# Kernel optimization log

Measured on AMD Instinct MI355X. Metric: run time of the kernel, lower is better.

Reference implementation:

```python
import jax, jax.numpy as jnp
import numpy as np

N = 524288   # tokens (accounts)
D = 9        # num_prop_size
E = 2        # expert_size
H = 128      # expert MLP hidden
M = 32       # moe_out
O = 2        # output_size
K = 1        # top-k
LOSS_COF = 0.01
EPS = 1e-10


def setup_inputs() -> dict:
    key = jax.random.key(0)
    ks = jax.random.split(key, 10)
    f32 = jnp.float32
    return {
        "num_prop": jax.random.normal(ks[0], (N, D), f32),
        "cat_prop": jax.random.normal(ks[1], (N, 3), f32),
        "w_gate": jax.random.normal(ks[2], (D, E), f32) * 0.1,
        "W1": jax.random.normal(ks[3], (E, D, H), f32) * 0.1,
        "b1": jax.random.normal(ks[4], (E, H), f32) * 0.01,
        "W2": jax.random.normal(ks[5], (E, H, M), f32) * 0.1,
        "b2": jax.random.normal(ks[6], (E, M), f32) * 0.01,
        "Wout": jax.random.normal(ks[7], (M, O), f32) * 0.1,
        "bout": jax.random.normal(ks[8], (O,), f32) * 0.01,
        "k": K,
    }


def _cv_squared(x):
    # torch: x.var() (unbiased) / (x.mean()**2 + eps)
    return jnp.var(x, ddof=1) / (jnp.mean(x) ** 2 + EPS)


def reference(num_prop, cat_prop, w_gate, W1, b1, W2, b2, Wout, bout, k):
    x = num_prop                                   # eval mode: dropout = identity
    n, e = x.shape[0], w_gate.shape[1]

    # --- top-k gating (eval: clean logits, no noise) ---
    logits = x @ w_gate                            # [N, E]
    top_logits, top_idx = jax.lax.top_k(logits, min(k + 1, e))
    top_k_gates = jax.nn.softmax(top_logits[:, :k], axis=1)   # [N, k]
    rows = jnp.arange(n)[:, None]
    gates = jnp.zeros_like(logits).at[rows, top_idx[:, :k]].set(top_k_gates)  # [N, E]

    importance = gates.sum(axis=0)                 # [E]
    load = (gates > 0).astype(jnp.float32).sum(axis=0)  # [E]
    loss = (_cv_squared(importance) + _cv_squared(load)) * LOSS_COF

    # --- experts: per-expert 2-layer MLP, computed dense (E=2) then gated combine ---
    h = jax.nn.relu(jnp.einsum("nd,edh->neh", x, W1) + b1)    # [N, E, H]
    y_e = jnp.einsum("neh,ehm->nem", h, W2) + b2              # [N, E, M]
    y = jnp.einsum("ne,nem->nm", gates, y_e)                  # [N, M]

    out = y @ Wout + bout                                     # [N, O]
    return (out, loss)
```

## Files before the change

kernel.cpp:

```cpp
#include <hip/hip_runtime.h>
#include <hip/hip_bf16.h>

#define NTOK 524288
#define TPB  256
#define NBLK (NTOK / TPB)

__device__ __forceinline__ float bf2f(unsigned short u) {
    union { unsigned int i; float f; } v;
    v.i = ((unsigned int)u) << 16;
    return v.f;
}

__device__ __forceinline__ float ldq(const void* p, int i, bool f32) {
    if (f32) return ((const float*)p)[i];
    return bf2f(((const unsigned short*)p)[i]);
}

__global__ void prep_kernel(const void* __restrict__ num_prop,
                            const void* __restrict__ wgate,
                            const void* __restrict__ W1,
                            const void* __restrict__ b1,
                            const void* __restrict__ W2,
                            const void* __restrict__ b2,
                            const void* __restrict__ Wout,
                            const void* __restrict__ bout,
                            unsigned int* __restrict__ cnt1,
                            int* __restrict__ flag,
                            float* __restrict__ bpp,
                            float* __restrict__ wgf,
                            float* __restrict__ wpack)
{
    __shared__ int sflag;
    const int t = threadIdx.x;
    if (t == 0) {
        const unsigned short* u = (const unsigned short*)num_prop;
        int f = 0;
        for (int i = 0; i < 72; ++i) {
            int e = (u[i] >> 7) & 0xFF;
            if (e < 64 || e > 191) f = 1;
        }
        sflag = f; *flag = f; *cnt1 = 0u;
    }
    __syncthreads();
    const bool f32 = (sflag != 0);

    if (t < 18) wgf[t] = ldq(wgate, t, f32);

    if (t < 4) {
        int e = t >> 1, o = t & 1;
        float acc = ldq(bout, o, f32);
        for (int m = 0; m < 32; ++m)
            acc += ldq(b2, e * 32 + m, f32) * ldq(Wout, m * 2 + o, f32);
        bpp[t] = acc;
    }

    const int e = t >> 7;
    const int j = t & 127;
    float p0 = 0.f, p1 = 0.f;
    for (int m = 0; m < 32; ++m) {
        float w = ldq(W2, (e * 128 + j) * 32 + m, f32);
        p0 += w * ldq(Wout, m * 2 + 0, f32);
        p1 += w * ldq(Wout, m * 2 + 1, f32);
    }
    float* dst = wpack + j * 24 + e * 12;
    #pragma unroll
    for (int d = 0; d < 9; ++d)
        dst[d] = ldq(W1, (e * 9 + d) * 128 + j, f32);
    dst[9]  = ldq(b1, e * 128 + j, f32);
    dst[10] = p0;
    dst[11] = p1;
}

__global__ __launch_bounds__(TPB, 8)
void moe_main(const void* __restrict__ xg,
              const int* __restrict__ flag,
              const float* __restrict__ wgf,
              const float* __restrict__ bpp,
              const float* __restrict__ wpack,
              unsigned int* __restrict__ cnt1,
              float2* __restrict__ out)
{
    __shared__ float xs[TPB * 9];
    __shared__ unsigned int cblk;
    const int tid = threadIdx.x;
    if (tid == 0) cblk = 0u;

    const bool f32 = (*flag) != 0;
    const int base = blockIdx.x * (TPB * 9);
    if (f32) {
        const float* xf = (const float*)xg;
        for (int i = tid; i < TPB * 9; i += TPB)
            xs[i] = xf[base + i];
    } else {
        const unsigned short* xu = (const unsigned short*)xg;
        for (int i = tid; i < TPB * 9; i += TPB)
            xs[i] = bf2f(xu[base + i]);
    }
    __syncthreads();

    float x[9];
    #pragma unroll
    for (int d = 0; d < 9; ++d) x[d] = xs[tid * 9 + d];

    float l0 = 0.f, l1 = 0.f;
    #pragma unroll
    for (int d = 0; d < 9; ++d) {
        l0 = fmaf(x[d], wgf[d * 2 + 0], l0);
        l1 = fmaf(x[d], wgf[d * 2 + 1], l1);
    }
    const bool e1 = l1 > l0;

    unsigned long long bal = __ballot(e1);
    if ((tid & 63) == 0)
        atomicAdd(&cblk, (unsigned int)__popcll(bal));

    float a00 = bpp[0], a01 = bpp[1], a10 = bpp[2], a11 = bpp[3];

    #pragma unroll 4
    for (int j = 0; j < 128; ++j) {
        const float* wp = wpack + j * 24;
        float h0 = wp[9], h1 = wp[21];
        #pragma unroll
        for (int d = 0; d < 9; ++d) {
            h0 = fmaf(x[d], wp[d],      h0);
            h1 = fmaf(x[d], wp[12 + d], h1);
        }
        h0 = fmaxf(h0, 0.f);
        h1 = fmaxf(h1, 0.f);
        a00 = fmaf(h0, wp[10], a00);
        a01 = fmaf(h0, wp[11], a01);
        a10 = fmaf(h1, wp[22], a10);
        a11 = fmaf(h1, wp[23], a11);
    }

    float2 o;
    o.x = e1 ? a10 : a00;
    o.y = e1 ? a11 : a01;
    out[blockIdx.x * TPB + tid] = o;

    __syncthreads();
    if (tid == 0) atomicAdd(cnt1, cblk);
}

__global__ void finalize_kernel(const unsigned int* __restrict__ cnt1,
                                float* __restrict__ loss_out)
{
    double c1 = (double)(*cnt1);
    double c0 = (double)NTOK - c1;
    double diff = c0 - c1;
    double mean = (double)NTOK * 0.5;
    double var  = 0.5 * diff * diff;
    double cv2  = var / (mean * mean + 1e-10);
    *loss_out = (float)(0.02 * cv2);
}

extern "C" void kernel_launch(void* const* d_in, const int* in_sizes, int n_in,
                              void* d_out, int out_size, void* d_ws, size_t ws_size,
                              hipStream_t stream) {
    const void* num_prop = d_in[0];
    const void* w_gate   = d_in[2];
    const void* W1       = d_in[3];
    const void* b1       = d_in[4];
    const void* W2       = d_in[5];
    const void* b2       = d_in[6];
    const void* Wout     = d_in[7];
    const void* bout     = d_in[8];

    char* ws = (char*)d_ws;
    unsigned int* cnt1 = (unsigned int*)ws;
    int* flag          = (int*)(ws + 8);
    float* bpp         = (float*)(ws + 16);
    float* wgf         = (float*)(ws + 64);
    float* wpack       = (float*)(ws + 192);

    float*  outf = (float*)d_out;
    float2* out2 = (float2*)d_out;

    hipLaunchKernelGGL(prep_kernel, dim3(1), dim3(256), 0, stream,
                       num_prop, w_gate, W1, b1, W2, b2, Wout, bout,
                       cnt1, flag, bpp, wgf, wpack);
    hipLaunchKernelGGL(moe_main, dim3(NBLK), dim3(TPB), 0, stream,
                       num_prop, flag, wgf, bpp, wpack, cnt1, out2);
    hipLaunchKernelGGL(finalize_kernel, dim3(1), dim3(1), 0, stream,
                       cnt1, outf + (size_t)NTOK * 2);
}
```

Before: 145.8 us.

## Sort tokens by expert within block to skip computing unused expert MLP

Tokens in each block are permuted by their top-1 expert through a ballot/mbcnt prefix, so most wavefronts hold tokens for a single expert and evaluate only that expert's MLP, roughly halving FLOPs. Mixed wavefronts fall back to computing both experts. The weight pack is split into per-expert contiguous arrays. The finalize kernel is folded into the main kernel with a last-block ticket counter, the input flag check is parallelised, and launch bounds drop to 6 blocks per SM. Risks are extra syncs, scattered output writes, and uniform weight loads from a different layout.

```diff
diff --git a/kernel.cpp b/kernel.cpp
--- a/kernel.cpp
+++ b/kernel.cpp
@@ -25,24 +25,24 @@
                             const void* __restrict__ Wout,
                             const void* __restrict__ bout,
                             unsigned int* __restrict__ cnt1,
+                            unsigned int* __restrict__ done,
                             int* __restrict__ flag,
                             float* __restrict__ bpp,
                             float* __restrict__ wgf,
                             float* __restrict__ wpack)
 {
-    __shared__ int sflag;
+    __shared__ int sbad;
     const int t = threadIdx.x;
-    if (t == 0) {
-        const unsigned short* u = (const unsigned short*)num_prop;
-        int f = 0;
-        for (int i = 0; i < 72; ++i) {
-            int e = (u[i] >> 7) & 0xFF;
-            if (e < 64 || e > 191) f = 1;
-        }
-        sflag = f; *flag = f; *cnt1 = 0u;
-    }
-    __syncthreads();
-    const bool f32 = (sflag != 0);
+    if (t == 0) { sbad = 0; *cnt1 = 0u; *done = 0u; }
+    __syncthreads();
+    if (t < 72) {
+        unsigned short u = ((const unsigned short*)num_prop)[t];
+        int e = (u >> 7) & 0xFF;
+        if (e < 64 || e > 191) sbad = 1;
+    }
+    __syncthreads();
+    const bool f32 = (sbad != 0);
+    if (t == 0) *flag = sbad;
 
     if (t < 18) wgf[t] = ldq(wgate, t, f32);
 
@@ -62,7 +62,7 @@
         p0 += w * ldq(Wout, m * 2 + 0, f32);
         p1 += w * ldq(Wout, m * 2 + 1, f32);
     }
-    float* dst = wpack + j * 24 + e * 12;
+    float* dst = wpack + e * 1536 + j * 12;
     #pragma unroll
     for (int d = 0; d < 9; ++d)
         dst[d] = ldq(W1, (e * 9 + d) * 128 + j, f32);
@@ -71,87 +71,125 @@
     dst[11] = p1;
 }
 
-__global__ __launch_bounds__(TPB, 8)
+__global__ __launch_bounds__(TPB, 6)
 void moe_main(const void* __restrict__ xg,
               const int* __restrict__ flag,
               const float* __restrict__ wgf,
               const float* __restrict__ bpp,
               const float* __restrict__ wpack,
               unsigned int* __restrict__ cnt1,
-              float2* __restrict__ out)
+              unsigned int* __restrict__ done,
+              float2* __restrict__ out,
+              float* __restrict__ loss_out)
 {
     __shared__ float xs[TPB * 9];
-    __shared__ unsigned int cblk;
-    const int tid = threadIdx.x;
-    if (tid == 0) cblk = 0u;
+    __shared__ unsigned short perm[TPB];
+    __shared__ int wcnt[4];
+    const int tid  = threadIdx.x;
+    const int lane = tid & 63;
+    const int wave = tid >> 6;
 
     const bool f32 = (*flag) != 0;
     const int base = blockIdx.x * (TPB * 9);
+    float xo[9];
     if (f32) {
-        const float* xf = (const float*)xg;
-        for (int i = tid; i < TPB * 9; i += TPB)
-            xs[i] = xf[base + i];
+        const float* xf = (const float*)xg + base + tid * 9;
+        #pragma unroll
+        for (int d = 0; d < 9; ++d) xo[d] = xf[d];
     } else {
-        const unsigned short* xu = (const unsigned short*)xg;
-        for (int i = tid; i < TPB * 9; i += TPB)
-            xs[i] = bf2f(xu[base + i]);
-    }
-    __syncthreads();
-
+        const unsigned short* xu = (const unsigned short*)xg + base + tid * 9;
+        #pragma unroll
+        for (int d = 0; d < 9; ++d) xo[d] = bf2f(xu[d]);
+    }
+    #pragma unroll
+    for (int d = 0; d < 9; ++d) xs[tid * 9 + d] = xo[d];
+
+    float l0 = 0.f, l1 = 0.f;
+    #pragma unroll
+    for (int d = 0; d < 9; ++d) {
+        l0 = fmaf(xo[d], wgf[d * 2 + 0], l0);
+        l1 = fmaf(xo[d], wgf[d * 2 + 1], l1);
+    }
+    const bool e1 = l1 > l0;
+
+    unsigned long long m1 = __ballot(e1);
+    int pre1 = __builtin_amdgcn_mbcnt_hi((unsigned)(m1 >> 32),
+               __builtin_amdgcn_mbcnt_lo((unsigned)m1, 0u));
+    if (lane == 0) wcnt[wave] = (int)__popcll(m1);
+    __syncthreads();
+    int w0 = wcnt[0], w1 = wcnt[1], w2 = wcnt[2], w3 = wcnt[3];
+    int c1_tot = w0 + w1 + w2 + w3;
+    int c0_tot = TPB - c1_tot;
+    int off1 = (wave > 0 ? w0 : 0) + (wave > 1 ? w1 : 0) + (wave > 2 ? w2 : 0);
+    int off0 = wave * 64 - off1;
+    int pos = e1 ? (c0_tot + off1 + pre1) : (off0 + (lane - pre1));
+    perm[pos] = (unsigned short)tid;
+    if (tid == 0) atomicAdd(cnt1, (unsigned int)c1_tot);
+    __syncthreads();
+
+    const int tok = perm[tid];
     float x[9];
     #pragma unroll
-    for (int d = 0; d < 9; ++d) x[d] = xs[tid * 9 + d];
-
-    float l0 = 0.f, l1 = 0.f;
-    #pragma unroll
-    for (int d = 0; d < 9; ++d) {
-        l0 = fmaf(x[d], wgf[d * 2 + 0], l0);
-        l1 = fmaf(x[d], wgf[d * 2 + 1], l1);
-    }
-    const bool e1 = l1 > l0;
-
-    unsigned long long bal = __ballot(e1);
-    if ((tid & 63) == 0)
-        atomicAdd(&cblk, (unsigned int)__popcll(bal));
-
-    float a00 = bpp[0], a01 = bpp[1], a10 = bpp[2], a11 = bpp[3];
-
-    #pragma unroll 4
-    for (int j = 0; j < 128; ++j) {
-        const float* wp = wpack + j * 24;
-        float h0 = wp[9], h1 = wp[21];
-        #pragma unroll
-        for (int d = 0; d < 9; ++d) {
-            h0 = fmaf(x[d], wp[d],      h0);
-            h1 = fmaf(x[d], wp[12 + d], h1);
+    for (int d = 0; d < 9; ++d) x[d] = xs[tok * 9 + d];
+    __syncthreads();
+
+    const bool my1 = (tid >= c0_tot);
+    unsigned long long bm = __ballot(my1);
+
+    float o0, o1;
+    if (bm == 0ull || bm == ~0ull) {
+        const int eb = (bm != 0ull) ? 1 : 0;
+        const float* wp = wpack + eb * 1536;
+        float a0 = bpp[eb * 2 + 0], a1 = bpp[eb * 2 + 1];
+        #pragma unroll 4
+        for (int j = 0; j < 128; ++j) {
+            const float* w = wp + j * 12;
+            float h = w[9];
+            #pragma unroll
+            for (int d = 0; d < 9; ++d) h = fmaf(x[d], w[d], h);
+            h = fmaxf(h, 0.f);
+            a0 = fmaf(h, w[10], a0);
+            a1 = fmaf(h, w[11], a1);
         }
-        h0 = fmaxf(h0, 0.f);
-        h1 = fmaxf(h1, 0.f);
-        a00 = fmaf(h0, wp[10], a00);
-        a01 = fmaf(h0, wp[11], a01);
-        a10 = fmaf(h1, wp[22], a10);
-        a11 = fmaf(h1, wp[23], a11);
-    }
-
-    float2 o;
-    o.x = e1 ? a10 : a00;
-    o.y = e1 ? a11 : a01;
-    out[blockIdx.x * TPB + tid] = o;
-
-    __syncthreads();
-    if (tid == 0) atomicAdd(cnt1, cblk);
-}
-
-__global__ void finalize_kernel(const unsigned int* __restrict__ cnt1,
-                                float* __restrict__ loss_out)
-{
-    double c1 = (double)(*cnt1);
-    double c0 = (double)NTOK - c1;
-    double diff = c0 - c1;
-    double mean = (double)NTOK * 0.5;
-    double var  = 0.5 * diff * diff;
-    double cv2  = var / (mean * mean + 1e-10);
-    *loss_out = (float)(0.02 * cv2);
+        o0 = a0; o1 = a1;
+    } else {
+        float a00 = bpp[0], a01 = bpp[1], a10 = bpp[2], a11 = bpp[3];
+        #pragma unroll 4
+        for (int j = 0; j < 128; ++j) {
+            const float* w0p = wpack + j * 12;
+            const float* w1p = wpack + 1536 + j * 12;
+            float h0 = w0p[9], h1 = w1p[9];
+            #pragma unroll
+            for (int d = 0; d < 9; ++d) {
+                h0 = fmaf(x[d], w0p[d], h0);
+                h1 = fmaf(x[d], w1p[d], h1);
+            }
+            h0 = fmaxf(h0, 0.f);
+            h1 = fmaxf(h1, 0.f);
+            a00 = fmaf(h0, w0p[10], a00);
+            a01 = fmaf(h0, w0p[11], a01);
+            a10 = fmaf(h1, w1p[10], a10);
+            a11 = fmaf(h1, w1p[11], a11);
+        }
+        o0 = my1 ? a10 : a00;
+        o1 = my1 ? a11 : a01;
+    }
+
+    float2 o; o.x = o0; o.y = o1;
+    out[blockIdx.x * TPB + tok] = o;
+
+    if (tid == 0) {
+        __threadfence();
+        unsigned int ticket = atomicAdd(done, 1u);
+        if (ticket == (unsigned int)(NBLK - 1)) {
+            double c1 = (double)atomicAdd(cnt1, 0u);
+            double c0 = (double)NTOK - c1;
+            double diff = c0 - c1;
+            double mean = (double)NTOK * 0.5;
+            double cv2  = (0.5 * diff * diff) / (mean * mean + 1e-10);
+            *loss_out = (float)(0.02 * cv2);
+        }
+    }
 }
 
 extern "C" void kernel_launch(void* const* d_in, const int* in_sizes, int n_in,
@@ -168,8 +206,9 @@
 
     char* ws = (char*)d_ws;
     unsigned int* cnt1 = (unsigned int*)ws;
+    unsigned int* done = (unsigned int*)(ws + 4);
     int* flag          = (int*)(ws + 8);
-    float* bpp         = (float*)(ws + 16);
+    float* bpp         = (float*)(ws + 32);
     float* wgf         = (float*)(ws + 64);
     float* wpack       = (float*)(ws + 192);
 
@@ -178,9 +217,8 @@
 
     hipLaunchKernelGGL(prep_kernel, dim3(1), dim3(256), 0, stream,
                        num_prop, w_gate, W1, b1, W2, b2, Wout, bout,
-                       cnt1, flag, bpp, wgf, wpack);
+                       cnt1, done, flag, bpp, wgf, wpack);
     hipLaunchKernelGGL(moe_main, dim3(NBLK), dim3(TPB), 0, stream,
-                       num_prop, flag, wgf, bpp, wpack, cnt1, out2);
-    hipLaunchKernelGGL(finalize_kernel, dim3(1), dim3(1), 0, stream,
-                       cnt1, outf + (size_t)NTOK * 2);
-}
+                       num_prop, flag, wgf, bpp, wpack, cnt1, done,
+                       out2, outf + (size_t)NTOK * 2);
+}
```

Result: slower. 185.5 us (+27.2%).
